# Kernel optimization log

Hardware: AMD Instinct MI355X
Metric: run time of the kernel (lower is better)

Reference implementation:

```python
import jax, jax.numpy as jnp
import numpy as np

B, S, D, H = 2, 2048, 2048, 16
HD = D // H  # 128


def setup_inputs() -> dict:
    key = jax.random.key(0)
    ks = jax.random.split(key, 5)
    scale = 0.02
    return {
        "hidden_states": jax.random.normal(ks[0], (B, S, D), dtype=jnp.float32),
        "Wqkv_w": jax.random.normal(ks[1], (3 * D, D), dtype=jnp.float32) * scale,
        "Wqkv_b": jax.random.normal(ks[2], (3 * D,), dtype=jnp.float32) * scale,
        "out_w": jax.random.normal(ks[3], (D, D), dtype=jnp.float32) * scale,
        "out_b": jax.random.normal(ks[4], (D,), dtype=jnp.float32) * scale,
    }


def reference(hidden_states, Wqkv_w, Wqkv_b, out_w, out_b):
    b, s, d = hidden_states.shape
    # QKV projection (torch Linear: x @ W.T + b)
    qkv = hidden_states @ Wqkv_w.T + Wqkv_b          # [b, s, 3d]
    qkv = qkv.reshape(b, s, 3, H, HD)                 # 'b s (three h d)'
    q, k, v = qkv[:, :, 0], qkv[:, :, 1], qkv[:, :, 2]  # [b, s, h, hd]
    softmax_scale = 1.0 / np.float32(np.sqrt(HD))
    # full quadratic scores, matching the naive baddbmm path
    scores = jnp.einsum('bthd,bshd->bhts', q, k) * softmax_scale  # [b,h,t,s]
    # causal=False (module default), dropout_p=0.0 -> no mask, no dropout
    attn = jax.nn.softmax(scores, axis=-1)
    ctx = jnp.einsum('bhts,bshd->bthd', attn, v)      # [b, t, h, hd]
    ctx = ctx.reshape(b, s, d)
    return ctx @ out_w.T + out_b
```

## Files before the change

### kernel.cpp

```cpp
#include <hip/hip_runtime.h>
#include <cstdint>
#include <cstddef>

#define B_ 2
#define S_ 2048
#define D_ 2048
#define H_ 16
#define HD_ 128
#define NTOK 4096
#define NQKV 6144

typedef unsigned short u16;
typedef __attribute__((ext_vector_type(8))) __bf16 bf16x8;
typedef __attribute__((ext_vector_type(4))) float f32x4;

__device__ __forceinline__ u16 f2bf(float f) {
  uint32_t u = __builtin_bit_cast(uint32_t, f);
  u = (u + 0x7FFFu + ((u >> 16) & 1u)) >> 16;
  return (u16)u;
}

__device__ __forceinline__ void gload_lds16(const void* g, void* l) {
  __builtin_amdgcn_global_load_lds(
      (const __attribute__((address_space(1))) void*)g,
      (__attribute__((address_space(3))) void*)l, 16, 0, 0);
}

__global__ void cvt_f32_bf16(const float* __restrict__ src, u16* __restrict__ dst, int n8) {
  int idx = blockIdx.x * blockDim.x + threadIdx.x;
  int stride = gridDim.x * blockDim.x;
  for (int i = idx; i < n8; i += stride) {
    const float4* s = (const float4*)(src + (size_t)i * 8);
    float4 a = s[0], b = s[1];
    union { u16 u[8]; uint4 v; } o;
    o.u[0] = f2bf(a.x); o.u[1] = f2bf(a.y); o.u[2] = f2bf(a.z); o.u[3] = f2bf(a.w);
    o.u[4] = f2bf(b.x); o.u[5] = f2bf(b.y); o.u[6] = f2bf(b.z); o.u[7] = f2bf(b.w);
    *(uint4*)(dst + (size_t)i * 8) = o.v;
  }
}

__device__ __forceinline__ void gemm_bt_tile(
    const u16* __restrict__ A, const u16* __restrict__ B,
    int lda, int ldb, int K, int m0, int n0,
    u16* As, u16* Bs, f32x4 acc[4][4])
{
  const int tid = threadIdx.x;
  const int lane = tid & 63;
  const int wid = tid >> 6;
  const int wr = wid >> 1, wc = wid & 1;
  const int fr = lane & 15, fq = lane >> 4;

  for (int k0 = 0; k0 < K; k0 += 32) {
    __syncthreads();
#pragma unroll
    for (int i = 0; i < 2; ++i) {
      int cbase = (i * 4 + wid) * 64;
      int c = cbase + lane;
      int r = c >> 2, c8 = (c & 3) * 8;
      gload_lds16(A + (size_t)(m0 + r) * lda + k0 + c8, As + (size_t)cbase * 8);
      gload_lds16(B + (size_t)(n0 + r) * ldb + k0 + c8, Bs + (size_t)cbase * 8);
    }
    __syncthreads();

    bf16x8 a[4], b[4];
#pragma unroll
    for (int m = 0; m < 4; ++m)
      a[m] = *(const bf16x8*)&As[(wr * 64 + m * 16 + fr) * 32 + fq * 8];
#pragma unroll
    for (int n = 0; n < 4; ++n)
      b[n] = *(const bf16x8*)&Bs[(wc * 64 + n * 16 + fr) * 32 + fq * 8];
#pragma unroll
    for (int m = 0; m < 4; ++m)
#pragma unroll
      for (int n = 0; n < 4; ++n)
        acc[m][n] = __builtin_amdgcn_mfma_f32_16x16x32_bf16(a[m], b[n], acc[m][n], 0, 0, 0);
  }
}

__global__ __launch_bounds__(256) void qkv_gemm(
    const u16* __restrict__ hsb, const u16* __restrict__ wb,
    const float* __restrict__ bias,
    u16* __restrict__ qb, u16* __restrict__ kb, u16* __restrict__ vT)
{
  __shared__ alignas(16) u16 As[128 * 32];
  __shared__ alignas(16) u16 Bs[128 * 32];
  f32x4 acc[4][4];
  f32x4 z = {0.f, 0.f, 0.f, 0.f};
#pragma unroll
  for (int m = 0; m < 4; ++m)
#pragma unroll
    for (int n = 0; n < 4; ++n) acc[m][n] = z;

  int m0 = blockIdx.x * 128, n0 = blockIdx.y * 128;
  gemm_bt_tile(hsb, wb, D_, D_, D_, m0, n0, As, Bs, acc);

  const float qscale = 0.08838834764831845f;
  const int lane = threadIdx.x & 63;
  const int wid = threadIdx.x >> 6;
  const int wr = wid >> 1, wc = wid & 1;
  const int fr = lane & 15, fq = lane >> 4;
#pragma unroll
  for (int m = 0; m < 4; ++m)
#pragma unroll
    for (int n = 0; n < 4; ++n) {
      int col = n0 + wc * 64 + n * 16 + fr;
      float bv = bias[col];
      int t = col >> 11;
      int d2 = col & 2047;
      int h = d2 >> 7, hd = d2 & 127;
#pragma unroll
      for (int r = 0; r < 4; ++r) {
        int row = m0 + wr * 64 + m * 16 + fq * 4 + r;
        int bb = row >> 11, s = row & 2047;
        int bh = bb * H_ + h;
        float val = acc[m][n][r] + bv;
        if (t == 0)      qb[((size_t)bh * S_ + s) * HD_ + hd] = f2bf(val * qscale);
        else if (t == 1) kb[((size_t)bh * S_ + s) * HD_ + hd] = f2bf(val);
        else             vT[((size_t)bh * HD_ + hd) * S_ + s] = f2bf(val);
      }
    }
}

__global__ __launch_bounds__(256) void out_gemm(
    const u16* __restrict__ ctx, const u16* __restrict__ wo,
    const float* __restrict__ bias, float* __restrict__ out)
{
  __shared__ alignas(16) u16 As[128 * 32];
  __shared__ alignas(16) u16 Bs[128 * 32];
  f32x4 acc[4][4];
  f32x4 z = {0.f, 0.f, 0.f, 0.f};
#pragma unroll
  for (int m = 0; m < 4; ++m)
#pragma unroll
    for (int n = 0; n < 4; ++n) acc[m][n] = z;

  int m0 = blockIdx.x * 128, n0 = blockIdx.y * 128;
  gemm_bt_tile(ctx, wo, D_, D_, D_, m0, n0, As, Bs, acc);

  const int lane = threadIdx.x & 63;
  const int wid = threadIdx.x >> 6;
  const int wr = wid >> 1, wc = wid & 1;
  const int fr = lane & 15, fq = lane >> 4;
#pragma unroll
  for (int m = 0; m < 4; ++m)
#pragma unroll
    for (int n = 0; n < 4; ++n) {
      int col = n0 + wc * 64 + n * 16 + fr;
      float bv = bias[col];
#pragma unroll
      for (int r = 0; r < 4; ++r) {
        int row = m0 + wr * 64 + m * 16 + fq * 4 + r;
        out[(size_t)row * D_ + col] = acc[m][n][r] + bv;
      }
    }
}

__global__ __launch_bounds__(256, 2) void attn(
    const u16* __restrict__ qb, const u16* __restrict__ kb,
    const u16* __restrict__ vT, u16* __restrict__ ctx)
{
  __shared__ alignas(16) u16 Kl[64 * 128];
  __shared__ alignas(16) u16 Vl[128 * 64];
  __shared__ alignas(16) u16 Pl[4][32 * 64];

  const int tid = threadIdx.x, lane = tid & 63, wid = tid >> 6;
  const int fr = lane & 15, fq = lane >> 4;
  const int bh = blockIdx.y;
  const int q0 = blockIdx.x * 128 + wid * 32;
  f32x4 z = {0.f, 0.f, 0.f, 0.f};

  const u16* qbase = qb + ((size_t)bh * S_ + q0) * HD_;
  bf16x8 qa[2][4];
#pragma unroll
  for (int h = 0; h < 2; ++h)
#pragma unroll
    for (int kc = 0; kc < 4; ++kc)
      qa[h][kc] = *(const bf16x8*)(qbase + (size_t)(h * 16 + fr) * HD_ + kc * 32 + fq * 8);

  f32x4 accv[2][8];
#pragma unroll
  for (int h = 0; h < 2; ++h)
#pragma unroll
    for (int n = 0; n < 8; ++n) accv[h][n] = z;
  float m_run[2] = {-1e30f, -1e30f};
  float l_run[2] = {0.f, 0.f};

  const u16* Kg = kb + (size_t)bh * S_ * HD_;
  const u16* Vg = vT + (size_t)bh * HD_ * S_;

  for (int kv = 0; kv < S_; kv += 64) {
    __syncthreads();
#pragma unroll
    for (int i = 0; i < 4; ++i) {
      int c = i * 256 + tid;
      {
        int row = c >> 4, cc = c & 15;
        uint4 t4 = *(const uint4*)(Kg + (size_t)(kv + row) * HD_ + cc * 8);
        *(uint4*)&Kl[row * 128 + ((cc * 8) ^ ((row & 7) << 3))] = t4;
      }
      {
        int rv = c >> 3, cv = c & 7;
        uint4 v4 = *(const uint4*)(Vg + (size_t)rv * S_ + kv + cv * 8);
        *(uint4*)&Vl[rv * 64 + ((cv * 8) ^ ((rv & 7) << 3))] = v4;
      }
    }
    __syncthreads();

    f32x4 sc[2][4];
#pragma unroll
    for (int j = 0; j < 4; ++j) {
      f32x4 s0 = z, s1 = z;
#pragma unroll
      for (int kc = 0; kc < 4; ++kc) {
        int row = j * 16 + fr;
        bf16x8 kf = *(const bf16x8*)&Kl[row * 128 + ((kc * 32 + fq * 8) ^ ((row & 7) << 3))];
        s0 = __builtin_amdgcn_mfma_f32_16x16x32_bf16(kf, qa[0][kc], s0, 0, 0, 0);
        s1 = __builtin_amdgcn_mfma_f32_16x16x32_bf16(kf, qa[1][kc], s1, 0, 0, 0);
      }
      sc[0][j] = s0; sc[1][j] = s1;
    }

    float pmax[2];
#pragma unroll
    for (int h = 0; h < 2; ++h) {
      float mx = sc[h][0][0];
#pragma unroll
      for (int j = 0; j < 4; ++j)
#pragma unroll
        for (int r = 0; r < 4; ++r) mx = fmaxf(mx, sc[h][j][r]);
      mx = fmaxf(mx, __shfl_xor(mx, 16));
      mx = fmaxf(mx, __shfl_xor(mx, 32));
      pmax[h] = mx;
    }

    int need = (pmax[0] > m_run[0] + 8.f) || (pmax[1] > m_run[1] + 8.f);
    if (__any(need)) {
#pragma unroll
      for (int h = 0; h < 2; ++h) {
        float mn = fmaxf(m_run[h], pmax[h]);
        float corr = __expf(m_run[h] - mn);
        m_run[h] = mn;
        l_run[h] *= corr;
#pragma unroll
        for (int r = 0; r < 4; ++r) {
          float rc = __shfl(corr, (lane & 48) | (fq * 4 + r));
#pragma unroll
          for (int n = 0; n < 8; ++n) accv[h][n][r] *= rc;
        }
      }
    }

    u16* Pw = Pl[wid];
#pragma unroll
    for (int h = 0; h < 2; ++h) {
      float ls = 0.f;
#pragma unroll
      for (int j = 0; j < 4; ++j) {
        union { u16 u[4]; ushort4 v; } pk;
#pragma unroll
        for (int r = 0; r < 4; ++r) {
          float p = __expf(sc[h][j][r] - m_run[h]);
          ls += p;
          pk.u[r] = f2bf(p);
        }
        int prow = h * 16 + fr;
        *(ushort4*)&Pw[prow * 64 + ((j * 16 + fq * 4) ^ ((fr & 7) << 3))] = pk.v;
      }
      ls += __shfl_xor(ls, 16);
      ls += __shfl_xor(ls, 32);
      l_run[h] += ls;
    }

#pragma unroll
    for (int kc = 0; kc < 2; ++kc) {
      int pcol = (kc * 32 + fq * 8) ^ ((fr & 7) << 3);
      bf16x8 pa0 = *(const bf16x8*)&Pw[fr * 64 + pcol];
      bf16x8 pa1 = *(const bf16x8*)&Pw[(16 + fr) * 64 + pcol];
#pragma unroll
      for (int n = 0; n < 8; ++n) {
        int row = n * 16 + fr;
        bf16x8 vf = *(const bf16x8*)&Vl[row * 64 + ((kc * 32 + fq * 8) ^ ((row & 7) << 3))];
        accv[0][n] = __builtin_amdgcn_mfma_f32_16x16x32_bf16(pa0, vf, accv[0][n], 0, 0, 0);
        accv[1][n] = __builtin_amdgcn_mfma_f32_16x16x32_bf16(pa1, vf, accv[1][n], 0, 0, 0);
      }
    }
  }

  float inv[2][4];
#pragma unroll
  for (int h = 0; h < 2; ++h)
#pragma unroll
    for (int r = 0; r < 4; ++r) {
      float l = __shfl(l_run[h], (lane & 48) | (fq * 4 + r));
      inv[h][r] = 1.f / l;
    }
  u16* cb = ctx + (((size_t)(bh >> 4)) * S_ + blockIdx.x * 128 + wid * 32) * D_ + (size_t)(bh & 15) * HD_;
#pragma unroll
  for (int h = 0; h < 2; ++h)
#pragma unroll
    for (int n = 0; n < 8; ++n)
#pragma unroll
      for (int r = 0; r < 4; ++r) {
        int q = h * 16 + fq * 4 + r;
        cb[(size_t)q * D_ + n * 16 + fr] = f2bf(accv[h][n][r] * inv[h][r]);
      }
}

extern "C" void kernel_launch(void* const* d_in, const int* in_sizes, int n_in,
                              void* d_out, int out_size, void* d_ws, size_t ws_size,
                              hipStream_t stream) {
  const float* hs   = (const float*)d_in[0];
  const float* wqkv = (const float*)d_in[1];
  const float* bqkv = (const float*)d_in[2];
  const float* wo   = (const float*)d_in[3];
  const float* bo   = (const float*)d_in[4];
  float* out = (float*)d_out;

  char* ws = (char*)d_ws;
  u16* hsb   = (u16*)(ws);
  u16* wqkvb = (u16*)(ws + 16777216);
  u16* wob   = (u16*)(ws + 41943040);
  u16* qb    = (u16*)(ws + 50331648);
  u16* kb    = (u16*)(ws + 67108864);
  u16* vT    = (u16*)(ws + 83886080);
  u16* ctx   = (u16*)(ws + 100663296);

  cvt_f32_bf16<<<2048, 256, 0, stream>>>(hs,   hsb,   (B_ * S_ * D_) / 8);
  cvt_f32_bf16<<<2048, 256, 0, stream>>>(wqkv, wqkvb, (NQKV * D_) / 8);
  cvt_f32_bf16<<<1024, 256, 0, stream>>>(wo,   wob,   (D_ * D_) / 8);

  qkv_gemm<<<dim3(NTOK / 128, NQKV / 128), 256, 0, stream>>>(hsb, wqkvb, bqkv, qb, kb, vT);
  attn<<<dim3(S_ / 128, B_ * H_), 256, 0, stream>>>(qb, kb, vT, ctx);
  out_gemm<<<dim3(NTOK / 128, D_ / 128), 256, 0, stream>>>(ctx, wob, bo, out);
}
```

Before: 308.6 us.

## Rewrite QKV GEMM as 256x256 tile with double-buffered async LDS pipeline

Replaces the simple 128x128 QKV projection GEMM, which synchronizes twice per 32-wide k-step, with a 512-thread 256x256-tile kernel. It stages 64-wide k-slices into double-buffered, XOR-swizzled LDS using direct global-to-LDS loads, and interleaves those loads with MFMA phases under explicit vmcnt/lgkmcnt waits and priority hints. The aim is more data reuse per tile and hiding global-load latency behind matrix math. In exchange it uses 128KB of LDS, a large register footprint, and hand-scheduled barriers that are fragile to get right, and the grid drops to 16x24 blocks.

After: 327.9 us. +6.3%, slower.

```diff
diff --git a/kernel.cpp b/kernel.cpp
--- a/kernel.cpp
+++ b/kernel.cpp
@@ -39,6 +39,134 @@
   }
 }
 
+
+#define SBAR() do { asm volatile("" ::: "memory"); __builtin_amdgcn_s_barrier(); asm volatile("" ::: "memory"); } while (0)
+#define WLG0() do { asm volatile("s_waitcnt lgkmcnt(0)" ::: "memory"); __builtin_amdgcn_sched_barrier(0); } while (0)
+#define WVM(n) asm volatile("s_waitcnt vmcnt(" #n ")" ::: "memory")
+
+__device__ __forceinline__ void stage64(const u16* __restrict__ G, int grow0,
+                                        u16* ldsbase, int koff) {
+  const int tid = threadIdx.x;
+  const int r = tid >> 3, gp = tid & 7;
+  const int g = gp ^ (r & 7);
+  gload_lds16(G + (size_t)(grow0 + r) * D_ + koff + g * 8,
+              ldsbase + (tid >> 6) * 512);
+}
+
+#define STG_B0(buf,koff) do { stage64(Bp, n0,      sB + (buf)*16384,            (koff)); \
+                              stage64(Bp, n0+64,   sB + (buf)*16384 + 64*64,    (koff)); } while (0)
+#define STG_B1(buf,koff) do { stage64(Bp, n0+128,  sB + (buf)*16384 + 128*64,   (koff)); \
+                              stage64(Bp, n0+192,  sB + (buf)*16384 + 192*64,   (koff)); } while (0)
+#define STG_AX(buf,koff) do { stage64(Ap, m0,      sA + (buf)*16384,            (koff)); \
+                              stage64(Ap, m0+128,  sA + (buf)*16384 + 128*64,   (koff)); } while (0)
+#define STG_AY(buf,koff) do { stage64(Ap, m0+64,   sA + (buf)*16384 + 64*64,    (koff)); \
+                              stage64(Ap, m0+192,  sA + (buf)*16384 + 192*64,   (koff)); } while (0)
+
+#define LOADB(buf) do { \
+  _Pragma("unroll") for (int nf = 0; nf < 4; ++nf) \
+  _Pragma("unroll") for (int kk = 0; kk < 2; ++kk) \
+    breg[nf][kk] = *(const bf16x8*)(sB + (buf)*16384 + (wn*64 + nf*16 + fr)*64 + ((((kk<<2)|fq)^swz)<<3)); \
+} while (0)
+#define LOADA(buf,p) do { \
+  _Pragma("unroll") for (int mm = 0; mm < 2; ++mm) \
+  _Pragma("unroll") for (int kk = 0; kk < 2; ++kk) \
+    areg[mm][kk] = *(const bf16x8*)(sA + (buf)*16384 + (wm*128 + ((p)*2+mm)*16 + fr)*64 + ((((kk<<2)|fq)^swz)<<3)); \
+} while (0)
+#define MFMA16(p) do { __builtin_amdgcn_s_setprio(1); \
+  _Pragma("unroll") for (int mm = 0; mm < 2; ++mm) \
+  _Pragma("unroll") for (int nf = 0; nf < 4; ++nf) \
+  _Pragma("unroll") for (int kk = 0; kk < 2; ++kk) \
+    acc[(p)*2+mm][nf] = __builtin_amdgcn_mfma_f32_16x16x32_bf16(areg[mm][kk], breg[nf][kk], acc[(p)*2+mm][nf], 0, 0, 0); \
+  __builtin_amdgcn_s_setprio(0); } while (0)
+
+__device__ __forceinline__ void gemm256_loop(
+    const u16* __restrict__ Ap, const u16* __restrict__ Bp,
+    int m0, int n0, u16* sA, u16* sB, f32x4 acc[8][4])
+{
+  const int tid = threadIdx.x;
+  const int lane = tid & 63, wid = tid >> 6;
+  const int wm = wid >> 2, wn = wid & 3;
+  const int fr = lane & 15, fq = lane >> 4;
+  const int swz = fr & 7;
+  const int NI = D_ / 128;
+
+  bf16x8 breg[4][2];
+  bf16x8 areg[2][2];
+
+  STG_B0(0, 0); STG_B1(0, 0); STG_AX(0, 0); STG_AY(0, 0);
+  STG_B0(1, 64); STG_B1(1, 64); STG_AX(1, 64);
+  WVM(6);
+  SBAR();
+
+  for (int j = 0; j < NI - 1; ++j) {
+    const int kS = (2*j + 1) * 64;
+    const int kA = (2*j + 2) * 64;
+    const int kB = (2*j + 3) * 64;
+    LOADB(0); LOADA(0,0); STG_AY(1, kS); SBAR(); WLG0(); MFMA16(0); SBAR();
+    LOADA(0,1);           STG_B0(0, kA); SBAR(); WLG0(); MFMA16(1); SBAR();
+    LOADA(0,2);           STG_B1(0, kA); SBAR(); WLG0(); MFMA16(2); SBAR();
+    LOADA(0,3);           STG_AX(0, kA); SBAR(); WLG0(); MFMA16(3); WVM(6); SBAR();
+    LOADB(1); LOADA(1,0); STG_AY(0, kA); SBAR(); WLG0(); MFMA16(0); SBAR();
+    LOADA(1,1);           STG_B0(1, kB); SBAR(); WLG0(); MFMA16(1); SBAR();
+    LOADA(1,2);           STG_B1(1, kB); SBAR(); WLG0(); MFMA16(2); SBAR();
+    LOADA(1,3);           STG_AX(1, kB); SBAR(); WLG0(); MFMA16(3); WVM(6); SBAR();
+  }
+  {
+    const int kS = (2*NI - 1) * 64;
+    LOADB(0); LOADA(0,0); STG_AY(1, kS); SBAR(); WLG0(); MFMA16(0); SBAR();
+    LOADA(0,1);                          SBAR(); WLG0(); MFMA16(1); SBAR();
+    LOADA(0,2);                          SBAR(); WLG0(); MFMA16(2); SBAR();
+    LOADA(0,3);                          SBAR(); WLG0(); MFMA16(3); WVM(0); SBAR();
+    LOADB(1); LOADA(1,0);                SBAR(); WLG0(); MFMA16(0); SBAR();
+    LOADA(1,1);                          SBAR(); WLG0(); MFMA16(1); SBAR();
+    LOADA(1,2);                          SBAR(); WLG0(); MFMA16(2); SBAR();
+    LOADA(1,3);                          SBAR(); WLG0(); MFMA16(3); SBAR();
+  }
+}
+
+__global__ __launch_bounds__(512, 2) void qkv_gemm(
+    const u16* __restrict__ hsb, const u16* __restrict__ wb,
+    const float* __restrict__ bias,
+    u16* __restrict__ qb, u16* __restrict__ kb, u16* __restrict__ vT)
+{
+  __shared__ alignas(1024) u16 sA[2 * 16384];
+  __shared__ alignas(1024) u16 sB[2 * 16384];
+  f32x4 acc[8][4];
+  f32x4 z = {0.f, 0.f, 0.f, 0.f};
+#pragma unroll
+  for (int m = 0; m < 8; ++m)
+#pragma unroll
+    for (int n = 0; n < 4; ++n) acc[m][n] = z;
+
+  const int m0 = blockIdx.x * 256, n0 = blockIdx.y * 256;
+  gemm256_loop(hsb, wb, m0, n0, sA, sB, acc);
+
+  const float qscale = 0.08838834764831845f;
+  const int lane = threadIdx.x & 63, wid = threadIdx.x >> 6;
+  const int wm = wid >> 2, wn = wid & 3;
+  const int fr = lane & 15, fq = lane >> 4;
+  const int t = (n0 + wn * 64) >> 11;
+#pragma unroll
+  for (int mf = 0; mf < 8; ++mf)
+#pragma unroll
+    for (int nf = 0; nf < 4; ++nf) {
+      int col = n0 + wn * 64 + nf * 16 + fr;
+      float bv = bias[col];
+      int d2 = col & 2047;
+      int h = d2 >> 7, hd = d2 & 127;
+#pragma unroll
+      for (int r = 0; r < 4; ++r) {
+        int row = m0 + wm * 128 + mf * 16 + fq * 4 + r;
+        int bb = row >> 11, s = row & 2047;
+        int bh = bb * H_ + h;
+        float val = acc[mf][nf][r] + bv;
+        if (t == 0)      qb[((size_t)bh * S_ + s) * HD_ + hd] = f2bf(val * qscale);
+        else if (t == 1) kb[((size_t)bh * S_ + s) * HD_ + hd] = f2bf(val);
+        else             vT[((size_t)bh * HD_ + hd) * S_ + s] = f2bf(val);
+      }
+    }
+}
+
 __device__ __forceinline__ void gemm_bt_tile(
     const u16* __restrict__ A, const u16* __restrict__ B,
     int lda, int ldb, int K, int m0, int n0,
@@ -77,50 +205,6 @@
   }
 }
 
-__global__ __launch_bounds__(256) void qkv_gemm(
-    const u16* __restrict__ hsb, const u16* __restrict__ wb,
-    const float* __restrict__ bias,
-    u16* __restrict__ qb, u16* __restrict__ kb, u16* __restrict__ vT)
-{
-  __shared__ alignas(16) u16 As[128 * 32];
-  __shared__ alignas(16) u16 Bs[128 * 32];
-  f32x4 acc[4][4];
-  f32x4 z = {0.f, 0.f, 0.f, 0.f};
-#pragma unroll
-  for (int m = 0; m < 4; ++m)
-#pragma unroll
-    for (int n = 0; n < 4; ++n) acc[m][n] = z;
-
-  int m0 = blockIdx.x * 128, n0 = blockIdx.y * 128;
-  gemm_bt_tile(hsb, wb, D_, D_, D_, m0, n0, As, Bs, acc);
-
-  const float qscale = 0.08838834764831845f;
-  const int lane = threadIdx.x & 63;
-  const int wid = threadIdx.x >> 6;
-  const int wr = wid >> 1, wc = wid & 1;
-  const int fr = lane & 15, fq = lane >> 4;
-#pragma unroll
-  for (int m = 0; m < 4; ++m)
-#pragma unroll
-    for (int n = 0; n < 4; ++n) {
-      int col = n0 + wc * 64 + n * 16 + fr;
-      float bv = bias[col];
-      int t = col >> 11;
-      int d2 = col & 2047;
-      int h = d2 >> 7, hd = d2 & 127;
-#pragma unroll
-      for (int r = 0; r < 4; ++r) {
-        int row = m0 + wr * 64 + m * 16 + fq * 4 + r;
-        int bb = row >> 11, s = row & 2047;
-        int bh = bb * H_ + h;
-        float val = acc[m][n][r] + bv;
-        if (t == 0)      qb[((size_t)bh * S_ + s) * HD_ + hd] = f2bf(val * qscale);
-        else if (t == 1) kb[((size_t)bh * S_ + s) * HD_ + hd] = f2bf(val);
-        else             vT[((size_t)bh * HD_ + hd) * S_ + s] = f2bf(val);
-      }
-    }
-}
-
 __global__ __launch_bounds__(256) void out_gemm(
     const u16* __restrict__ ctx, const u16* __restrict__ wo,
     const float* __restrict__ bias, float* __restrict__ out)
@@ -329,7 +413,7 @@
   cvt_f32_bf16<<<2048, 256, 0, stream>>>(wqkv, wqkvb, (NQKV * D_) / 8);
   cvt_f32_bf16<<<1024, 256, 0, stream>>>(wo,   wob,   (D_ * D_) / 8);
 
-  qkv_gemm<<<dim3(NTOK / 128, NQKV / 128), 256, 0, stream>>>(hsb, wqkvb, bqkv, qb, kb, vT);
+  qkv_gemm<<<dim3(NTOK / 256, NQKV / 256), 512, 0, stream>>>(hsb, wqkvb, bqkv, qb, kb, vT);
   attn<<<dim3(S_ / 128, B_ * H_), 256, 0, stream>>>(qb, kb, vT, ctx);
   out_gemm<<<dim3(NTOK / 128, D_ / 128), 256, 0, stream>>>(ctx, wob, bo, out);
 }
```
